# Kernel optimization log

Hardware: AMD Instinct MI355X
Metric: run time of the kernel (lower is better)

Reference implementation:

```python
import jax, jax.numpy as jnp
import numpy as np

VOCAB = 50000
D = 32            # hidden_size
OUT = 5           # output_size (sentiment classes)
B = 512           # number of balanced trees
L = 64            # leaves per tree (power of 2)


def setup_inputs() -> dict:
    key = jax.random.key(0)
    ks = jax.random.split(key, 6)
    # scale params down to avoid tanh saturation (original uses xavier init)
    return {
        "word_ids": jax.random.randint(ks[0], (B, L), 0, VOCAB, dtype=jnp.int32),
        "embed": jax.random.normal(ks[1], (VOCAB, D), jnp.float32) * 0.1,
        "V": jax.random.normal(ks[2], (D, 2 * D, 2 * D), jnp.float32) * 0.02,
        "W": jax.random.normal(ks[3], (2 * D, D), jnp.float32) * 0.1,
        "b": jnp.zeros((1, D), jnp.float32),
        "Wout_w": jax.random.normal(ks[4], (OUT, D), jnp.float32) * 0.1,
        "Wout_b": jnp.zeros((OUT,), jnp.float32),
    }


def reference(word_ids, embed, V, W, b, Wout_w, Wout_b):
    # Leaves: embedding lookup. h: [B, n_nodes_at_level, D]
    h = embed[word_ids]                              # [B, L, D]
    all_nodes = [h.reshape(-1, D)]
    n_levels = int(np.log2(h.shape[1]))
    for _ in range(n_levels):
        left = h[:, 0::2]                            # [B, n/2, D]
        right = h[:, 1::2]                           # [B, n/2, D]
        c = jnp.concatenate([left, right], axis=-1)  # [B, n/2, 2D]
        # xVx_k = c @ V_k @ c^T for each slice k of the tensor V
        Vc = jnp.einsum('kjl,bnl->bnkj', V, c)       # [B, n/2, D, 2D]
        xVx = jnp.einsum('bnj,bnkj->bnk', c, Vc)     # [B, n/2, D]
        h = jnp.tanh(xVx + c @ W + b)                # [B, n/2, D]
        all_nodes.append(h.reshape(-1, D))
    nodes = jnp.concatenate(all_nodes, axis=0)       # [B*(2L-1), D]
    logits = nodes @ Wout_w.T + Wout_b               # [B*(2L-1), OUT]
    log_probs = jax.nn.log_softmax(logits, axis=-1)
    roots = h[:, 0, :]                               # [B, D]
    return log_probs, roots
```

## Files before the change

kernel.cpp:

```cpp
#include <hip/hip_runtime.h>

#define OUT_N 5
#define TOTAL_NODES 65024
#define ROOTS_OFF (TOTAL_NODES * OUT_N)
#define NLEAF 32768

typedef __attribute__((ext_vector_type(8))) short bf16x8;
typedef __attribute__((ext_vector_type(4))) float f32x4;
typedef __attribute__((ext_vector_type(8))) unsigned short ushort8v;
typedef __attribute__((ext_vector_type(4))) unsigned int uint4v;

static __device__ __forceinline__ float bf2f(unsigned short u) {
    union { unsigned int i; float f; } v; v.i = ((unsigned int)u) << 16; return v.f;
}
static __device__ __forceinline__ unsigned short f2bf(float f) {
    union { float f; unsigned int i; } v; v.f = f;
    unsigned int r = v.i + 0x7fff + ((v.i >> 16) & 1);
    return (unsigned short)(r >> 16);
}
static __device__ __forceinline__ int node_addr(int R, int q) {
    return R * 64 + (((q ^ ((R >> 1) & 3)) & 3) << 4);
}

__global__ __launch_bounds__(64) void bprep_kernel(
    const float* __restrict__ V, const float* __restrict__ W,
    unsigned short* __restrict__ B)
{
    int t = blockIdx.x * 64 + threadIdx.x;
    if (t >= 8576) return;
    int ks = t >> 7, sub = t & 127;
    int n = sub >> 6, lane = sub & 63;
    int hi = lane >> 4, l15 = lane & 15;
    int k = n * 16 + l15;
    const float* Vk = V + (size_t)k * 4096;
    ushort8v o;
    #pragma unroll
    for (int i = 0; i < 8; ++i) {
        int r5 = hi * 8 + i;
        float val;
        if (ks < 2)        { int j = 32 * ks + r5; val = Vk[j * 64 + j]; }
        else if (ks < 64)  { int d = ks >> 1; int j = 32 * (ks & 1) + r5; int l = (j + d) & 63;
                             val = Vk[j * 64 + l] + Vk[l * 64 + j]; }
        else if (ks == 64) { int j = r5; val = Vk[j * 64 + j + 32] + Vk[(j + 32) * 64 + j]; }
        else               { int j = (ks == 65) ? r5 : (32 + r5); val = W[j * 32 + k]; }
        o[i] = f2bf(val);
    }
    *(ushort8v*)(B + (size_t)t * 8) = o;
}

static __device__ __forceinline__ void load_crot(
    const char* nodes, int Rc, int hi, float* crot)
{
    #pragma unroll
    for (int t = 0; t < 8; ++t) {
        int m = (hi + t) & 7;
        ushort8v v = *(const ushort8v*)(nodes + node_addr(Rc + (m >> 2), m & 3));
        #pragma unroll
        for (int e = 0; e < 8; ++e) crot[t * 8 + e] = bf2f(v[e]);
    }
}

template<int K0, int K1>
static __device__ __forceinline__ f32x4 run1_k(
    const unsigned short* __restrict__ Bg, const float* crot,
    int lane, int n, f32x4 acc)
{
    const char* bp = (const char*)Bg + lane * 16 + (n << 10);
    #pragma unroll
    for (int ks = K0; ks < K1; ++ks) {
        uint4v aw;
        #pragma unroll
        for (int q = 0; q < 4; ++q) {
            int i0 = 2 * q, i1 = 2 * q + 1;
            float p0, p1;
            if (ks < 2)       { p0 = crot[32*ks+i0] * crot[32*ks+i0];
                                p1 = crot[32*ks+i1] * crot[32*ks+i1]; }
            else if (ks < 64) { const int bse = 32 * (ks & 1), d = ks >> 1;
                                p0 = crot[bse+i0] * crot[(bse+i0+d)&63];
                                p1 = crot[bse+i1] * crot[(bse+i1+d)&63]; }
            else if (ks == 64){ p0 = crot[i0] * crot[32+i0];
                                p1 = crot[i1] * crot[32+i1]; }
            else if (ks == 65){ p0 = crot[i0];    p1 = crot[i1]; }
            else              { p0 = crot[32+i0]; p1 = crot[32+i1]; }
            unsigned int pk;
            asm("v_cvt_pk_bf16_f32 %0, %1, %2" : "=v"(pk) : "v"(p0), "v"(p1));
            aw[q] = pk;
        }
        bf16x8 afr = __builtin_bit_cast(bf16x8, aw);
        bf16x8 bfr = *(const bf16x8*)(bp + (ks << 11));
        acc = __builtin_amdgcn_mfma_f32_16x16x32_bf16(afr, bfr, acc, 0, 0, 0);
    }
    return acc;
}

__global__ __launch_bounds__(256, 4) void l1_kernel(
    const int* __restrict__ word_ids, const float* __restrict__ embed,
    const unsigned short* __restrict__ Bg, const float* __restrict__ bias,
    unsigned short* __restrict__ h1)
{
    __shared__ char smem[2048 + 2048];
    const int tid = threadIdx.x, lane = tid & 63;
    const int l15 = lane & 15, hi = lane >> 4, wave = tid >> 6;
    const int n = wave >> 1, u = wave & 1;
    const int tile = blockIdx.x;

    {
        int rr = tid >> 3, q4 = tid & 7;
        int r = rr >> 1, child = rr & 1;
        int g1 = tile * 16 + r;
        int leaf = (g1 >> 5) * 64 + (g1 & 31) * 2 + child;
        int wid = word_ids[leaf];
        float4 v = ((const float4*)(embed + (size_t)wid * 32))[q4];
        uint2 st;
        st.x = (unsigned)f2bf(v.x) | ((unsigned)f2bf(v.y) << 16);
        st.y = (unsigned)f2bf(v.z) | ((unsigned)f2bf(v.w) << 16);
        *(uint2*)(smem + node_addr(rr, q4 >> 1) + (q4 & 1) * 8) = st;
    }
    __syncthreads();

    float crot[64];
    load_crot(smem, 2 * l15, hi, crot);

    f32x4 acc = { 0.f, 0.f, 0.f, 0.f };
    if (u == 0) acc = run1_k<0, 34>(Bg, crot, lane, n, acc);
    else        acc = run1_k<34, 67>(Bg, crot, lane, n, acc);

    if (u == 1) *(f32x4*)(smem + 2048 + n * 1024 + lane * 16) = acc;
    __syncthreads();
    if (u == 0) {
        acc += *(const f32x4*)(smem + 2048 + n * 1024 + lane * 16);
        float bk = bias[n * 16 + l15];
        #pragma unroll
        for (int r = 0; r < 4; ++r) {
            int node = tile * 16 + hi * 4 + r;
            h1[(size_t)node * 32 + n * 16 + l15] = f2bf(tanhf(acc[r] + bk));
        }
    }
}

constexpr int SCR = 8192;

template<int RPT, int CHILDB, int OUTB, int OG, bool ROOT>
static __device__ __forceinline__ void level_deep(
    char* smem, const unsigned short* __restrict__ Bg,
    const float* __restrict__ bias, unsigned short* __restrict__ hbuf,
    float* __restrict__ roots, int bid, int lane, int wave)
{
    const int l15 = lane & 15, hi = lane >> 4;
    const int n = wave >> 2, u = wave & 3;

    int rc = (l15 < 2 * RPT) ? l15 : 0;
    int tree = rc / RPT, i = rc % RPT;
    float crot[64];
    load_crot(smem, tree * 64 + CHILDB + 2 * i, hi, crot);

    f32x4 acc = { 0.f, 0.f, 0.f, 0.f };
    switch (u) {
        case 0:  acc = run1_k< 0, 17>(Bg, crot, lane, n, acc); break;
        case 1:  acc = run1_k<17, 34>(Bg, crot, lane, n, acc); break;
        case 2:  acc = run1_k<34, 50>(Bg, crot, lane, n, acc); break;
        default: acc = run1_k<50, 67>(Bg, crot, lane, n, acc); break;
    }
    if (u > 0) *(f32x4*)(smem + SCR + (n * 3 + u - 1) * 1024 + lane * 16) = acc;
    __syncthreads();
    if (u == 0) {
        #pragma unroll
        for (int v2 = 0; v2 < 3; ++v2)
            acc += *(const f32x4*)(smem + SCR + (n * 3 + v2) * 1024 + lane * 16);
        float bk = bias[n * 16 + l15];
        int col = n * 16 + l15;
        #pragma unroll
        for (int r4 = 0; r4 < 4; ++r4) {
            int row = hi * 4 + r4;
            if (row < 2 * RPT) {
                float h = tanhf(acc[r4] + bk);
                unsigned short hb = f2bf(h);
                int t2 = row / RPT, i2 = row % RPT;
                *(unsigned short*)(smem + node_addr(t2 * 64 + OUTB + i2, col >> 3) + (col & 7) * 2) = hb;
                hbuf[((size_t)OG + (size_t)(bid * 2 + t2) * RPT + i2) * 32 + col] = hb;
                if (ROOT) roots[(size_t)(bid * 2 + t2) * 32 + col] = h;
            }
        }
    }
    __syncthreads();
}

__global__ __launch_bounds__(512, 2) void tail_kernel(
    const unsigned short* __restrict__ Bg, const float* __restrict__ bias,
    unsigned short* __restrict__ hbuf, float* __restrict__ roots)
{
    __shared__ char smem[8192 + 6144];
    const int tid = threadIdx.x, lane = tid & 63;
    const int l15 = lane & 15, hi = lane >> 4, wave = tid >> 6;
    const int bid = blockIdx.x;

    if (tid < 256) {
        int nr = tid >> 2, q = tid & 3;
        int t = nr >> 5, i = nr & 31;
        ushort8v v = *(const ushort8v*)(hbuf + ((size_t)(bid * 2 + t) * 32 + i) * 32 + q * 8);
        *(ushort8v*)(smem + node_addr(t * 64 + i, q)) = v;
    }
    __syncthreads();

    {
        const int t = wave >> 2, n = (wave >> 1) & 1, u = wave & 1;
        float crot[64];
        load_crot(smem, t * 64 + 2 * l15, hi, crot);
        f32x4 acc = { 0.f, 0.f, 0.f, 0.f };
        if (u == 0) acc = run1_k<0, 34>(Bg, crot, lane, n, acc);
        else        acc = run1_k<34, 67>(Bg, crot, lane, n, acc);
        if (u == 1) *(f32x4*)(smem + SCR + (t * 2 + n) * 1024 + lane * 16) = acc;
        __syncthreads();
        if (u == 0) {
            acc += *(const f32x4*)(smem + SCR + (t * 2 + n) * 1024 + lane * 16);
            float bk = bias[n * 16 + l15];
            int col = n * 16 + l15;
            #pragma unroll
            for (int r4 = 0; r4 < 4; ++r4) {
                int row = hi * 4 + r4;
                float h = tanhf(acc[r4] + bk);
                unsigned short hb = f2bf(h);
                *(unsigned short*)(smem + node_addr(t * 64 + 32 + row, col >> 3) + (col & 7) * 2) = hb;
                hbuf[((size_t)16384 + (size_t)(bid * 2 + t) * 16 + row) * 32 + col] = hb;
            }
        }
        __syncthreads();
    }

    level_deep<8, 32, 48, 24576, false>(smem, Bg, bias, hbuf, roots, bid, lane, wave);
    level_deep<4, 48, 56, 28672, false>(smem, Bg, bias, hbuf, roots, bid, lane, wave);
    level_deep<2, 56, 60, 30720, false>(smem, Bg, bias, hbuf, roots, bid, lane, wave);
    level_deep<1, 60, 62, 31744, true >(smem, Bg, bias, hbuf, roots, bid, lane, wave);
}

__global__ __launch_bounds__(256) void out_kernel(
    const int* __restrict__ word_ids, const float* __restrict__ embed,
    const unsigned short* __restrict__ hbuf,
    const float* __restrict__ Wout_w, const float* __restrict__ Wout_b,
    float* __restrict__ out)
{
    int g = blockIdx.x * 256 + threadIdx.x;
    if (g >= TOTAL_NODES) return;

    float h[32];
    if (g < NLEAF) {
        int wid = word_ids[g];
        const float4* p = (const float4*)(embed + (size_t)wid * 32);
        #pragma unroll
        for (int q = 0; q < 8; ++q) {
            float4 v = p[q];
            h[q*4] = v.x; h[q*4+1] = v.y; h[q*4+2] = v.z; h[q*4+3] = v.w;
        }
    } else {
        const ushort8v* p = (const ushort8v*)(hbuf + (size_t)(g - NLEAF) * 32);
        #pragma unroll
        for (int q = 0; q < 4; ++q) {
            ushort8v v = p[q];
            #pragma unroll
            for (int e = 0; e < 8; ++e) h[q*8+e] = bf2f(v[e]);
        }
    }

    float logits[OUT_N];
    #pragma unroll
    for (int o = 0; o < OUT_N; ++o) {
        const float* w = Wout_w + o * 32;
        float s = 0.f;
        #pragma unroll
        for (int x = 0; x < 32; ++x) s = fmaf(w[x], h[x], s);
        logits[o] = s + Wout_b[o];
    }
    float m = logits[0];
    #pragma unroll
    for (int o = 1; o < OUT_N; ++o) m = fmaxf(m, logits[o]);
    float sum = 0.f;
    #pragma unroll
    for (int o = 0; o < OUT_N; ++o) sum += expf(logits[o] - m);
    float lse = m + logf(sum);
    #pragma unroll
    for (int o = 0; o < OUT_N; ++o) out[(size_t)g * OUT_N + o] = logits[o] - lse;
}

extern "C" void kernel_launch(void* const* d_in, const int* in_sizes, int n_in,
                              void* d_out, int out_size, void* d_ws, size_t ws_size,
                              hipStream_t stream)
{
    const int*   word_ids = (const int*)  d_in[0];
    const float* embed    = (const float*)d_in[1];
    const float* V        = (const float*)d_in[2];
    const float* W        = (const float*)d_in[3];
    const float* bvec     = (const float*)d_in[4];
    const float* Wout_w   = (const float*)d_in[5];
    const float* Wout_b   = (const float*)d_in[6];
    float* out = (float*)d_out;

    unsigned short* Bfrag = (unsigned short*)d_ws;
    unsigned short* hbuf  = (unsigned short*)((char*)d_ws + 137216);
    float* roots = out + ROOTS_OFF;

    bprep_kernel<<<134, 64, 0, stream>>>(V, W, Bfrag);
    l1_kernel<<<1024, 256, 0, stream>>>(word_ids, embed, Bfrag, bvec, hbuf);
    tail_kernel<<<256, 512, 0, stream>>>(Bfrag, bvec, hbuf, roots);
    out_kernel<<<254, 256, 0, stream>>>(word_ids, embed, hbuf, Wout_w, Wout_b, out);
}
```

Measured before the change: 34.51 us.

## Fuse output log-softmax into tree kernels, keep hidden states fp32 in LDS

Removes the separate out_kernel. Leaf log-softmax is computed in l1_kernel using shuffles, and internal-node logits are computed from shared memory in l1 and tail kernels, so the hbuf round trip for higher levels is gone. Hidden states are kept in fp32 with a new swizzled LDS layout instead of bf16. Each wave now computes both 16-column halves with two MFMAs, and the K range is split across more waves (4 in l1, 8 in deep levels). The trade-off is higher LDS use and h1 traffic that is now fp32. The logits tail runs on only a few threads per block, which may serialize.

```diff
diff --git a/kernel.cpp b/kernel.cpp
--- a/kernel.cpp
+++ b/kernel.cpp
@@ -3,23 +3,23 @@
 #define OUT_N 5
 #define TOTAL_NODES 65024
 #define ROOTS_OFF (TOTAL_NODES * OUT_N)
-#define NLEAF 32768
 
 typedef __attribute__((ext_vector_type(8))) short bf16x8;
 typedef __attribute__((ext_vector_type(4))) float f32x4;
 typedef __attribute__((ext_vector_type(8))) unsigned short ushort8v;
 typedef __attribute__((ext_vector_type(4))) unsigned int uint4v;
 
-static __device__ __forceinline__ float bf2f(unsigned short u) {
-    union { unsigned int i; float f; } v; v.i = ((unsigned int)u) << 16; return v.f;
-}
 static __device__ __forceinline__ unsigned short f2bf(float f) {
     union { float f; unsigned int i; } v; v.f = f;
     unsigned int r = v.i + 0x7fff + ((v.i >> 16) & 1);
     return (unsigned short)(r >> 16);
 }
-static __device__ __forceinline__ int node_addr(int R, int q) {
-    return R * 64 + (((q ^ ((R >> 1) & 3)) & 3) << 4);
+
+static __device__ __forceinline__ int naddr32(int R, int c) {
+    return R * 128 + (((c + R) & 7) << 4);
+}
+static __device__ __forceinline__ void store_h32(char* smem, int R, int col, float v) {
+    *(float*)(smem + naddr32(R, col >> 2) + (col & 3) * 4) = v;
 }
 
 __global__ __launch_bounds__(64) void bprep_kernel(
@@ -48,24 +48,25 @@
     *(ushort8v*)(B + (size_t)t * 8) = o;
 }
 
-static __device__ __forceinline__ void load_crot(
+static __device__ __forceinline__ void load_crot32(
     const char* nodes, int Rc, int hi, float* crot)
 {
     #pragma unroll
-    for (int t = 0; t < 8; ++t) {
-        int m = (hi + t) & 7;
-        ushort8v v = *(const ushort8v*)(nodes + node_addr(Rc + (m >> 2), m & 3));
-        #pragma unroll
-        for (int e = 0; e < 8; ++e) crot[t * 8 + e] = bf2f(v[e]);
+    for (int t = 0; t < 16; ++t) {
+        int m = (hi * 2 + t) & 15;
+        int row = Rc + (m >> 3), c4 = m & 7;
+        f32x4 v = *(const f32x4*)(nodes + naddr32(row, c4));
+        #pragma unroll
+        for (int e = 0; e < 4; ++e) crot[t * 4 + e] = v[e];
     }
 }
 
 template<int K0, int K1>
-static __device__ __forceinline__ f32x4 run1_k(
+static __device__ __forceinline__ void run2_k(
     const unsigned short* __restrict__ Bg, const float* crot,
-    int lane, int n, f32x4 acc)
-{
-    const char* bp = (const char*)Bg + lane * 16 + (n << 10);
+    int lane, f32x4& a0, f32x4& a1)
+{
+    const char* bp = (const char*)Bg + lane * 16;
     #pragma unroll
     for (int ks = K0; ks < K1; ++ks) {
         uint4v aw;
@@ -87,21 +88,53 @@
             aw[q] = pk;
         }
         bf16x8 afr = __builtin_bit_cast(bf16x8, aw);
-        bf16x8 bfr = *(const bf16x8*)(bp + (ks << 11));
-        acc = __builtin_amdgcn_mfma_f32_16x16x32_bf16(afr, bfr, acc, 0, 0, 0);
-    }
-    return acc;
+        bf16x8 b0 = *(const bf16x8*)(bp + (ks << 11));
+        bf16x8 b1 = *(const bf16x8*)(bp + (ks << 11) + 1024);
+        a0 = __builtin_amdgcn_mfma_f32_16x16x32_bf16(afr, b0, a0, 0, 0, 0);
+        a1 = __builtin_amdgcn_mfma_f32_16x16x32_bf16(afr, b1, a1, 0, 0, 0);
+    }
+}
+
+static __device__ __forceinline__ void node_logits32(
+    const char* smem, int R, const float* __restrict__ Wout_w,
+    const float* __restrict__ Wout_b, float* __restrict__ out, size_t g)
+{
+    float h[32];
+    #pragma unroll
+    for (int c = 0; c < 8; ++c) {
+        f32x4 v = *(const f32x4*)(smem + naddr32(R, c));
+        #pragma unroll
+        for (int e = 0; e < 4; ++e) h[c * 4 + e] = v[e];
+    }
+    float lg[OUT_N];
+    #pragma unroll
+    for (int o = 0; o < OUT_N; ++o) {
+        const float* w = Wout_w + o * 32;
+        float s = 0.f;
+        #pragma unroll
+        for (int x = 0; x < 32; ++x) s = fmaf(w[x], h[x], s);
+        lg[o] = s + Wout_b[o];
+    }
+    float m = lg[0];
+    #pragma unroll
+    for (int o = 1; o < OUT_N; ++o) m = fmaxf(m, lg[o]);
+    float sum = 0.f;
+    #pragma unroll
+    for (int o = 0; o < OUT_N; ++o) sum += expf(lg[o] - m);
+    float lse = m + logf(sum);
+    #pragma unroll
+    for (int o = 0; o < OUT_N; ++o) out[g * OUT_N + o] = lg[o] - lse;
 }
 
 __global__ __launch_bounds__(256, 4) void l1_kernel(
     const int* __restrict__ word_ids, const float* __restrict__ embed,
     const unsigned short* __restrict__ Bg, const float* __restrict__ bias,
-    unsigned short* __restrict__ h1)
-{
-    __shared__ char smem[2048 + 2048];
+    const float* __restrict__ Wout_w, const float* __restrict__ Wout_b,
+    float* __restrict__ h1buf, float* __restrict__ out)
+{
+    __shared__ char smem[6144 + 6144];
     const int tid = threadIdx.x, lane = tid & 63;
-    const int l15 = lane & 15, hi = lane >> 4, wave = tid >> 6;
-    const int n = wave >> 1, u = wave & 1;
+    const int l15 = lane & 15, hi = lane >> 4, u = tid >> 6;
     const int tile = blockIdx.x;
 
     {
@@ -110,75 +143,127 @@
         int g1 = tile * 16 + r;
         int leaf = (g1 >> 5) * 64 + (g1 & 31) * 2 + child;
         int wid = word_ids[leaf];
-        float4 v = ((const float4*)(embed + (size_t)wid * 32))[q4];
-        uint2 st;
-        st.x = (unsigned)f2bf(v.x) | ((unsigned)f2bf(v.y) << 16);
-        st.y = (unsigned)f2bf(v.z) | ((unsigned)f2bf(v.w) << 16);
-        *(uint2*)(smem + node_addr(rr, q4 >> 1) + (q4 & 1) * 8) = st;
+        f32x4 v = ((const f32x4*)(embed + (size_t)wid * 32))[q4];
+        *(f32x4*)(smem + naddr32(rr, q4)) = v;
+
+        float lg[OUT_N];
+        #pragma unroll
+        for (int o = 0; o < OUT_N; ++o) {
+            const float* w = Wout_w + o * 32 + q4 * 4;
+            lg[o] = w[0]*v[0] + w[1]*v[1] + w[2]*v[2] + w[3]*v[3];
+        }
+        #pragma unroll
+        for (int o = 0; o < OUT_N; ++o) {
+            lg[o] += __shfl_xor(lg[o], 1, 64);
+            lg[o] += __shfl_xor(lg[o], 2, 64);
+            lg[o] += __shfl_xor(lg[o], 4, 64);
+        }
+        if (q4 == 0) {
+            #pragma unroll
+            for (int o = 0; o < OUT_N; ++o) lg[o] += Wout_b[o];
+            float m = lg[0];
+            #pragma unroll
+            for (int o = 1; o < OUT_N; ++o) m = fmaxf(m, lg[o]);
+            float sum = 0.f;
+            #pragma unroll
+            for (int o = 0; o < OUT_N; ++o) sum += expf(lg[o] - m);
+            float lse = m + logf(sum);
+            #pragma unroll
+            for (int o = 0; o < OUT_N; ++o) out[(size_t)leaf * OUT_N + o] = lg[o] - lse;
+        }
     }
     __syncthreads();
 
     float crot[64];
-    load_crot(smem, 2 * l15, hi, crot);
-
-    f32x4 acc = { 0.f, 0.f, 0.f, 0.f };
-    if (u == 0) acc = run1_k<0, 34>(Bg, crot, lane, n, acc);
-    else        acc = run1_k<34, 67>(Bg, crot, lane, n, acc);
-
-    if (u == 1) *(f32x4*)(smem + 2048 + n * 1024 + lane * 16) = acc;
+    load_crot32(smem, 2 * l15, hi, crot);
+
+    f32x4 a0 = {0.f,0.f,0.f,0.f}, a1 = {0.f,0.f,0.f,0.f};
+    if      (u == 0) run2_k< 0, 17>(Bg, crot, lane, a0, a1);
+    else if (u == 1) run2_k<17, 34>(Bg, crot, lane, a0, a1);
+    else if (u == 2) run2_k<34, 50>(Bg, crot, lane, a0, a1);
+    else             run2_k<50, 67>(Bg, crot, lane, a0, a1);
+
+    if (u > 0) {
+        char* sp = smem + 6144 + (u - 1) * 2048 + lane * 32;
+        *(f32x4*)sp = a0; *((f32x4*)sp + 1) = a1;
+    }
     __syncthreads();
     if (u == 0) {
-        acc += *(const f32x4*)(smem + 2048 + n * 1024 + lane * 16);
-        float bk = bias[n * 16 + l15];
+        #pragma unroll
+        for (int v2 = 0; v2 < 3; ++v2) {
+            const char* sp = smem + 6144 + v2 * 2048 + lane * 32;
+            a0 += *(const f32x4*)sp;
+            a1 += *((const f32x4*)sp + 1);
+        }
+        float bk0 = bias[l15], bk1 = bias[16 + l15];
         #pragma unroll
         for (int r = 0; r < 4; ++r) {
-            int node = tile * 16 + hi * 4 + r;
-            h1[(size_t)node * 32 + n * 16 + l15] = f2bf(tanhf(acc[r] + bk));
-        }
-    }
-}
-
-constexpr int SCR = 8192;
-
-template<int RPT, int CHILDB, int OUTB, int OG, bool ROOT>
+            int row = hi * 4 + r;
+            int node = tile * 16 + row;
+            float h0 = tanhf(a0[r] + bk0), h1v = tanhf(a1[r] + bk1);
+            h1buf[(size_t)node * 32 + l15]      = h0;
+            h1buf[(size_t)node * 32 + 16 + l15] = h1v;
+            store_h32(smem, 32 + row, l15, h0);
+            store_h32(smem, 32 + row, 16 + l15, h1v);
+        }
+    }
+    __syncthreads();
+    if (tid < 16)
+        node_logits32(smem, 32 + tid, Wout_w, Wout_b, out,
+                      (size_t)32768 + tile * 16 + tid);
+}
+
+constexpr int SCR_T = 16384;
+
+template<int RPT, int CHILDB, int OUTB, bool ROOT>
 static __device__ __forceinline__ void level_deep(
     char* smem, const unsigned short* __restrict__ Bg,
-    const float* __restrict__ bias, unsigned short* __restrict__ hbuf,
-    float* __restrict__ roots, int bid, int lane, int wave)
+    const float* __restrict__ bias, float* __restrict__ roots,
+    int bid, int lane, int wave)
 {
     const int l15 = lane & 15, hi = lane >> 4;
-    const int n = wave >> 2, u = wave & 3;
-
     int rc = (l15 < 2 * RPT) ? l15 : 0;
     int tree = rc / RPT, i = rc % RPT;
     float crot[64];
-    load_crot(smem, tree * 64 + CHILDB + 2 * i, hi, crot);
-
-    f32x4 acc = { 0.f, 0.f, 0.f, 0.f };
-    switch (u) {
-        case 0:  acc = run1_k< 0, 17>(Bg, crot, lane, n, acc); break;
-        case 1:  acc = run1_k<17, 34>(Bg, crot, lane, n, acc); break;
-        case 2:  acc = run1_k<34, 50>(Bg, crot, lane, n, acc); break;
-        default: acc = run1_k<50, 67>(Bg, crot, lane, n, acc); break;
-    }
-    if (u > 0) *(f32x4*)(smem + SCR + (n * 3 + u - 1) * 1024 + lane * 16) = acc;
-    __syncthreads();
-    if (u == 0) {
-        #pragma unroll
-        for (int v2 = 0; v2 < 3; ++v2)
-            acc += *(const f32x4*)(smem + SCR + (n * 3 + v2) * 1024 + lane * 16);
-        float bk = bias[n * 16 + l15];
-        int col = n * 16 + l15;
+    load_crot32(smem, tree * 64 + CHILDB + 2 * i, hi, crot);
+
+    f32x4 a0 = {0.f,0.f,0.f,0.f}, a1 = {0.f,0.f,0.f,0.f};
+    switch (wave) {
+        case 0:  run2_k< 0,  9>(Bg, crot, lane, a0, a1); break;
+        case 1:  run2_k< 9, 17>(Bg, crot, lane, a0, a1); break;
+        case 2:  run2_k<17, 26>(Bg, crot, lane, a0, a1); break;
+        case 3:  run2_k<26, 34>(Bg, crot, lane, a0, a1); break;
+        case 4:  run2_k<34, 42>(Bg, crot, lane, a0, a1); break;
+        case 5:  run2_k<42, 50>(Bg, crot, lane, a0, a1); break;
+        case 6:  run2_k<50, 59>(Bg, crot, lane, a0, a1); break;
+        default: run2_k<59, 67>(Bg, crot, lane, a0, a1); break;
+    }
+    if (wave > 0) {
+        char* sp = smem + SCR_T + (wave - 1) * 2048 + lane * 32;
+        *(f32x4*)sp = a0; *((f32x4*)sp + 1) = a1;
+    }
+    __syncthreads();
+    if (wave == 0) {
+        #pragma unroll
+        for (int v2 = 0; v2 < 7; ++v2) {
+            const char* sp = smem + SCR_T + v2 * 2048 + lane * 32;
+            a0 += *(const f32x4*)sp;
+            a1 += *((const f32x4*)sp + 1);
+        }
+        float bk0 = bias[l15], bk1 = bias[16 + l15];
         #pragma unroll
         for (int r4 = 0; r4 < 4; ++r4) {
             int row = hi * 4 + r4;
             if (row < 2 * RPT) {
-                float h = tanhf(acc[r4] + bk);
-                unsigned short hb = f2bf(h);
+                float h0 = tanhf(a0[r4] + bk0), h1v = tanhf(a1[r4] + bk1);
                 int t2 = row / RPT, i2 = row % RPT;
-                *(unsigned short*)(smem + node_addr(t2 * 64 + OUTB + i2, col >> 3) + (col & 7) * 2) = hb;
-                hbuf[((size_t)OG + (size_t)(bid * 2 + t2) * RPT + i2) * 32 + col] = hb;
-                if (ROOT) roots[(size_t)(bid * 2 + t2) * 32 + col] = h;
+                int R2 = t2 * 64 + OUTB + i2;
+                store_h32(smem, R2, l15, h0);
+                store_h32(smem, R2, 16 + l15, h1v);
+                if (ROOT) {
+                    roots[(size_t)(bid * 2 + t2) * 32 + l15]      = h0;
+                    roots[(size_t)(bid * 2 + t2) * 32 + 16 + l15] = h1v;
+                }
             }
         }
     }
@@ -187,98 +272,75 @@
 
 __global__ __launch_bounds__(512, 2) void tail_kernel(
     const unsigned short* __restrict__ Bg, const float* __restrict__ bias,
-    unsigned short* __restrict__ hbuf, float* __restrict__ roots)
-{
-    __shared__ char smem[8192 + 6144];
+    const float* __restrict__ h1buf,
+    const float* __restrict__ Wout_w, const float* __restrict__ Wout_b,
+    float* __restrict__ out)
+{
+    __shared__ char smem[16384 + 14336];
     const int tid = threadIdx.x, lane = tid & 63;
     const int l15 = lane & 15, hi = lane >> 4, wave = tid >> 6;
     const int bid = blockIdx.x;
-
-    if (tid < 256) {
-        int nr = tid >> 2, q = tid & 3;
-        int t = nr >> 5, i = nr & 31;
-        ushort8v v = *(const ushort8v*)(hbuf + ((size_t)(bid * 2 + t) * 32 + i) * 32 + q * 8);
-        *(ushort8v*)(smem + node_addr(t * 64 + i, q)) = v;
-    }
-    __syncthreads();
+    float* roots = out + ROOTS_OFF;
 
     {
-        const int t = wave >> 2, n = (wave >> 1) & 1, u = wave & 1;
+        int gRow = tid >> 3, c4 = tid & 7;
+        int t = gRow >> 5, i = gRow & 31;
+        f32x4 v = *(const f32x4*)(h1buf + ((size_t)(bid * 2 + t) * 32 + i) * 32 + c4 * 4);
+        *(f32x4*)(smem + naddr32(t * 64 + i, c4)) = v;
+    }
+    __syncthreads();
+
+    {
+        const int t = wave >> 2, u = wave & 3;
         float crot[64];
-        load_crot(smem, t * 64 + 2 * l15, hi, crot);
-        f32x4 acc = { 0.f, 0.f, 0.f, 0.f };
-        if (u == 0) acc = run1_k<0, 34>(Bg, crot, lane, n, acc);
-        else        acc = run1_k<34, 67>(Bg, crot, lane, n, acc);
-        if (u == 1) *(f32x4*)(smem + SCR + (t * 2 + n) * 1024 + lane * 16) = acc;
+        load_crot32(smem, t * 64 + 2 * l15, hi, crot);
+        f32x4 a0 = {0.f,0.f,0.f,0.f}, a1 = {0.f,0.f,0.f,0.f};
+        if      (u == 0) run2_k< 0, 17>(Bg, crot, lane, a0, a1);
+        else if (u == 1) run2_k<17, 34>(Bg, crot, lane, a0, a1);
+        else if (u == 2) run2_k<34, 50>(Bg, crot, lane, a0, a1);
+        else             run2_k<50, 67>(Bg, crot, lane, a0, a1);
+        if (u > 0) {
+            char* sp = smem + SCR_T + (t * 3 + u - 1) * 2048 + lane * 32;
+            *(f32x4*)sp = a0; *((f32x4*)sp + 1) = a1;
+        }
         __syncthreads();
         if (u == 0) {
-            acc += *(const f32x4*)(smem + SCR + (t * 2 + n) * 1024 + lane * 16);
-            float bk = bias[n * 16 + l15];
-            int col = n * 16 + l15;
+            #pragma unroll
+            for (int v2 = 0; v2 < 3; ++v2) {
+                const char* sp = smem + SCR_T + (t * 3 + v2) * 2048 + lane * 32;
+                a0 += *(const f32x4*)sp;
+                a1 += *((const f32x4*)sp + 1);
+            }
+            float bk0 = bias[l15], bk1 = bias[16 + l15];
             #pragma unroll
             for (int r4 = 0; r4 < 4; ++r4) {
                 int row = hi * 4 + r4;
-                float h = tanhf(acc[r4] + bk);
-                unsigned short hb = f2bf(h);
-                *(unsigned short*)(smem + node_addr(t * 64 + 32 + row, col >> 3) + (col & 7) * 2) = hb;
-                hbuf[((size_t)16384 + (size_t)(bid * 2 + t) * 16 + row) * 32 + col] = hb;
+                int R2 = t * 64 + 32 + row;
+                float h0 = tanhf(a0[r4] + bk0), h1v = tanhf(a1[r4] + bk1);
+                store_h32(smem, R2, l15, h0);
+                store_h32(smem, R2, 16 + l15, h1v);
             }
         }
         __syncthreads();
     }
 
-    level_deep<8, 32, 48, 24576, false>(smem, Bg, bias, hbuf, roots, bid, lane, wave);
-    level_deep<4, 48, 56, 28672, false>(smem, Bg, bias, hbuf, roots, bid, lane, wave);
-    level_deep<2, 56, 60, 30720, false>(smem, Bg, bias, hbuf, roots, bid, lane, wave);
-    level_deep<1, 60, 62, 31744, true >(smem, Bg, bias, hbuf, roots, bid, lane, wave);
-}
-
-__global__ __launch_bounds__(256) void out_kernel(
-    const int* __restrict__ word_ids, const float* __restrict__ embed,
-    const unsigned short* __restrict__ hbuf,
-    const float* __restrict__ Wout_w, const float* __restrict__ Wout_b,
-    float* __restrict__ out)
-{
-    int g = blockIdx.x * 256 + threadIdx.x;
-    if (g >= TOTAL_NODES) return;
-
-    float h[32];
-    if (g < NLEAF) {
-        int wid = word_ids[g];
-        const float4* p = (const float4*)(embed + (size_t)wid * 32);
-        #pragma unroll
-        for (int q = 0; q < 8; ++q) {
-            float4 v = p[q];
-            h[q*4] = v.x; h[q*4+1] = v.y; h[q*4+2] = v.z; h[q*4+3] = v.w;
-        }
-    } else {
-        const ushort8v* p = (const ushort8v*)(hbuf + (size_t)(g - NLEAF) * 32);
-        #pragma unroll
-        for (int q = 0; q < 4; ++q) {
-            ushort8v v = p[q];
-            #pragma unroll
-            for (int e = 0; e < 8; ++e) h[q*8+e] = bf2f(v[e]);
-        }
-    }
-
-    float logits[OUT_N];
-    #pragma unroll
-    for (int o = 0; o < OUT_N; ++o) {
-        const float* w = Wout_w + o * 32;
-        float s = 0.f;
-        #pragma unroll
-        for (int x = 0; x < 32; ++x) s = fmaf(w[x], h[x], s);
-        logits[o] = s + Wout_b[o];
-    }
-    float m = logits[0];
-    #pragma unroll
-    for (int o = 1; o < OUT_N; ++o) m = fmaxf(m, logits[o]);
-    float sum = 0.f;
-    #pragma unroll
-    for (int o = 0; o < OUT_N; ++o) sum += expf(logits[o] - m);
-    float lse = m + logf(sum);
-    #pragma unroll
-    for (int o = 0; o < OUT_N; ++o) out[(size_t)g * OUT_N + o] = logits[o] - lse;
+    level_deep<8, 32, 48, false>(smem, Bg, bias, roots, bid, lane, wave);
+    level_deep<4, 48, 56, false>(smem, Bg, bias, roots, bid, lane, wave);
+    level_deep<2, 56, 60, false>(smem, Bg, bias, roots, bid, lane, wave);
+    level_deep<1, 60, 62, true >(smem, Bg, bias, roots, bid, lane, wave);
+
+    if (tid < 62) {
+        int t = (tid >= 31) ? 1 : 0;
+        int rr = tid - 31 * t;
+        int R; size_t g;
+        int tg = bid * 2 + t;
+        if (rr < 16)      { R = t*64 + 32 + rr;        g = 49152 + (size_t)tg*16 + rr; }
+        else if (rr < 24) { R = t*64 + 48 + (rr-16);   g = 57344 + (size_t)tg*8  + (rr-16); }
+        else if (rr < 28) { R = t*64 + 56 + (rr-24);   g = 61440 + (size_t)tg*4  + (rr-24); }
+        else if (rr < 30) { R = t*64 + 60 + (rr-28);   g = 63488 + (size_t)tg*2  + (rr-28); }
+        else              { R = t*64 + 62;             g = 64512 + (size_t)tg; }
+        node_logits32(smem, R, Wout_w, Wout_b, out, g);
+    }
 }
 
 extern "C" void kernel_launch(void* const* d_in, const int* in_sizes, int n_in,
@@ -295,11 +357,10 @@
     float* out = (float*)d_out;
 
     unsigned short* Bfrag = (unsigned short*)d_ws;
-    unsigned short* hbuf  = (unsigned short*)((char*)d_ws + 137216);
-    float* roots = out + ROOTS_OFF;
+    float* h1buf = (float*)((char*)d_ws + 137216);
 
     bprep_kernel<<<134, 64, 0, stream>>>(V, W, Bfrag);
-    l1_kernel<<<1024, 256, 0, stream>>>(word_ids, embed, Bfrag, bvec, hbuf);
-    tail_kernel<<<256, 512, 0, stream>>>(Bfrag, bvec, hbuf, roots);
-    out_kernel<<<254, 256, 0, stream>>>(word_ids, embed, hbuf, Wout_w, Wout_b, out);
-}
+    l1_kernel<<<1024, 256, 0, stream>>>(word_ids, embed, Bfrag, bvec,
+                                        Wout_w, Wout_b, h1buf, out);
+    tail_kernel<<<256, 512, 0, stream>>>(Bfrag, bvec, h1buf, Wout_w, Wout_b, out);
+}
```

New measurement: 36.75 us. +6.5%, slower.
